# Performance work log

Hardware: AMD Instinct MI355X
Metric: run time of the kernel (lower is better)

The kernel has to match this reference:

```python
import jax, jax.numpy as jnp
import numpy as np
from jax import lax

B = 16
D_OUT = 1024      # flattened face-encoder latent
D_HID = 512       # config.mesh_conv.latent_channels
D_TEX = 16        # config.tex_features (output texture channels)
D_INTER = 32      # d_tex_inter
TEX = 256         # config.tex_dim
K = 3             # kernel_size
N0 = D_INTER * D_INTER * K * K   # first (inter->inter) filter size
N1 = D_TEX * D_INTER * K * K     # last (inter->tex) filter size
D_FLT9 = N0 + N1                 # = 13824


def setup_inputs() -> dict:
    key = jax.random.key(0)
    ks = jax.random.split(key, 8)
    return {
        "z_face": jax.random.normal(ks[0], (B, D_OUT), jnp.float32),
        "tex_data": jax.random.normal(ks[1], (1, D_INTER, TEX, TEX), jnp.float32),
        "W1": jax.random.normal(ks[2], (D_HID, D_OUT), jnp.float32) * 0.02,
        "b1": jnp.zeros((D_HID,), jnp.float32),
        "W2": jax.random.normal(ks[3], (D_HID, D_HID), jnp.float32) * 0.02,
        "b2": jnp.zeros((D_HID,), jnp.float32),
        "W3": jax.random.normal(ks[4], (D_FLT9, D_HID), jnp.float32) * 0.02,
        "b3": jnp.zeros((D_FLT9,), jnp.float32),
    }


def _lrelu(x):
    return jnp.where(x >= 0, x, 0.2 * x)


def reference(z_face, tex_data, W1, b1, W2, b2, W3, b3):
    # proj_w MLP: Linear -> LeakyReLU(0.2) -> Linear -> LeakyReLU(0.2) -> Linear
    h = _lrelu(z_face @ W1.T + b1)
    h = _lrelu(h @ W2.T + b2)
    weights = h @ W3.T + b3                      # [B, D_FLT9]

    flt0 = weights[:, :N0].reshape(B, D_INTER, D_INTER, K, K)   # inter->inter
    flt1 = weights[:, N0:].reshape(B, D_TEX, D_INTER, K, K)     # inter->tex

    pad_l = (K - 1) // 2
    pad_r = K - 1 - pad_l
    pad = [(pad_l, pad_r), (pad_l, pad_r)]

    def per_sample(w0, w1):
        # tex_data is shared across the batch (shape [1, D_INTER, TEX, TEX])
        x = lax.conv_general_dilated(tex_data, w0, (1, 1), pad)  # [1, D_INTER, TEX, TEX]
        x = _lrelu(x)
        x = lax.conv_general_dilated(x, w1, (1, 1), pad)         # [1, D_TEX, TEX, TEX]
        return x[0]

    out = jax.vmap(per_sample)(flt0, flt1)       # [B, D_TEX, TEX, TEX]
    return out
```

## Files before the change

kernel.cpp:

```cpp
#include <hip/hip_runtime.h>
#include <hip/hip_bf16.h>

#define BATCH 16
#define D_OUT 1024
#define D_HID 512
#define D_FLT 13824
#define N0Q 9216
#define TW 14
#define TH 14
#define NXT 19
#define NYT 19
#define NB 2

typedef __attribute__((ext_vector_type(8))) short bf16x8;
typedef __attribute__((ext_vector_type(4))) float f32x4;

__device__ __forceinline__ float lrelu(float x) { return x >= 0.f ? x : 0.2f * x; }
__device__ __forceinline__ ushort f2bf(float x) {
  unsigned u = __float_as_uint(x);
  u += 0x7FFFu + ((u >> 16) & 1u);
  return (ushort)(u >> 16);
}
__device__ __forceinline__ float dot4(float4 a, float4 b) {
  return a.x * b.x + a.y * b.y + a.z * b.z + a.w * b.w;
}
__device__ __forceinline__ bf16x8 cvt8(const float* p) {
  float4 lo = *(const float4*)p;
  float4 hi = *(const float4*)(p + 4);
  bf16x8 r;
  r[0] = (short)f2bf(lo.x); r[1] = (short)f2bf(lo.y);
  r[2] = (short)f2bf(lo.z); r[3] = (short)f2bf(lo.w);
  r[4] = (short)f2bf(hi.x); r[5] = (short)f2bf(hi.y);
  r[6] = (short)f2bf(hi.z); r[7] = (short)f2bf(hi.w);
  return r;
}

__global__ void fc1_tex_kernel(const float* __restrict__ z, const float* __restrict__ W1,
                               const float* __restrict__ b1, float* __restrict__ h1,
                               const float* __restrict__ tex, ushort* __restrict__ texT) {
  int tid = threadIdx.x;
  if (blockIdx.x < 256) {
    int p = blockIdx.x * 256 + tid;
    unsigned pk[16];
    #pragma unroll
    for (int i = 0; i < 16; ++i) {
      ushort lo = f2bf(tex[(2 * i) * 65536 + p]);
      ushort hi = f2bf(tex[(2 * i + 1) * 65536 + p]);
      pk[i] = (unsigned)lo | ((unsigned)hi << 16);
    }
    uint4* dst = (uint4*)&texT[(size_t)p * 32];
    #pragma unroll
    for (int qq = 0; qq < 4; ++qq) {
      uint4 v; v.x = pk[qq * 4]; v.y = pk[qq * 4 + 1]; v.z = pk[qq * 4 + 2]; v.w = pk[qq * 4 + 3];
      dst[qq] = v;
    }
    return;
  }
  int w = tid >> 6, lane = tid & 63;
  int wid = (blockIdx.x - 256) * 4 + w;
  int b = wid >> 7, j0 = (wid & 127) * 4;
  const float4* zv = (const float4*)(z + b * D_OUT);
  float4 zr[4];
  #pragma unroll
  for (int i = 0; i < 4; ++i) zr[i] = zv[lane + i * 64];
  float s[4];
  #pragma unroll
  for (int jj = 0; jj < 4; ++jj) {
    const float4* wv = (const float4*)(W1 + (j0 + jj) * D_OUT);
    float t = 0.f;
    #pragma unroll
    for (int i = 0; i < 4; ++i) t += dot4(zr[i], wv[lane + i * 64]);
    s[jj] = t;
  }
  #pragma unroll
  for (int jj = 0; jj < 4; ++jj) {
    #pragma unroll
    for (int off = 32; off; off >>= 1) s[jj] += __shfl_xor(s[jj], off);
  }
  if (lane == 0) {
    #pragma unroll
    for (int jj = 0; jj < 4; ++jj)
      h1[b * D_HID + j0 + jj] = lrelu(s[jj] + b1[j0 + jj]);
  }
}

__global__ void fc2_kernel(const float* __restrict__ in, const float* __restrict__ W,
                           const float* __restrict__ bias, float* __restrict__ out) {
  int tid = threadIdx.x;
  int w = tid >> 6, lane = tid & 63;
  int wid = blockIdx.x * 4 + w;
  int b = wid >> 7, j0 = (wid & 127) * 4;
  const float4* iv = (const float4*)(in + b * D_HID);
  float4 ir[2];
  #pragma unroll
  for (int i = 0; i < 2; ++i) ir[i] = iv[lane + i * 64];
  float s[4];
  #pragma unroll
  for (int jj = 0; jj < 4; ++jj) {
    const float4* wv = (const float4*)(W + (j0 + jj) * D_HID);
    float t = 0.f;
    #pragma unroll
    for (int i = 0; i < 2; ++i) t += dot4(ir[i], wv[lane + i * 64]);
    s[jj] = t;
  }
  #pragma unroll
  for (int jj = 0; jj < 4; ++jj) {
    #pragma unroll
    for (int off = 32; off; off >>= 1) s[jj] += __shfl_xor(s[jj], off);
  }
  if (lane == 0) {
    #pragma unroll
    for (int jj = 0; jj < 4; ++jj)
      out[b * D_HID + j0 + jj] = lrelu(s[jj] + bias[j0 + jj]);
  }
}

__global__ __launch_bounds__(256) void fc3_mfma(const float* __restrict__ h2,
                                                const float* __restrict__ W3,
                                                const float* __restrict__ b3,
                                                ushort* __restrict__ wbf) {
  const int tid = threadIdx.x;
  const int w = tid >> 6, lane = tid & 63;
  const int jn = lane & 15, q = lane >> 4;
  int t = blockIdx.x * 4 + w;
  int jbase, dstbase, ci0;
  if (t < 576) {
    int kp = t >> 6, rem = t & 63;
    int co = rem >> 1;
    ci0 = (rem & 1) * 16;
    jbase = co * 288 + kp;
    dstbase = kp * 1024 + co * 32 + ci0;
  } else {
    int t2 = t - 576;
    int kp = t2 >> 5, rem = t2 & 31;
    int co = rem >> 1;
    ci0 = (rem & 1) * 16;
    jbase = N0Q + co * 288 + kp;
    dstbase = N0Q + kp * 512 + co * 32 + ci0;
  }
  const float* wrow = W3 + (size_t)(jbase + (ci0 + jn) * 9) * D_HID;
  const float* hrow = h2 + jn * D_HID;
  f32x4 acc = {0.f, 0.f, 0.f, 0.f};
  #pragma unroll
  for (int ks = 0; ks < 16; ++ks) {
    int k0 = ks * 32 + q * 8;
    bf16x8 a = cvt8(wrow + k0);
    bf16x8 bv = cvt8(hrow + k0);
    acc = __builtin_amdgcn_mfma_f32_16x16x32_bf16(a, bv, acc, 0, 0, 0);
  }
  ushort4 o;
  o.x = f2bf(acc[0] + b3[jbase + (ci0 + q * 4 + 0) * 9]);
  o.y = f2bf(acc[1] + b3[jbase + (ci0 + q * 4 + 1) * 9]);
  o.z = f2bf(acc[2] + b3[jbase + (ci0 + q * 4 + 2) * 9]);
  o.w = f2bf(acc[3] + b3[jbase + (ci0 + q * 4 + 3) * 9]);
  *(ushort4*)&wbf[(size_t)jn * D_FLT + dstbase + q * 4] = o;
}

__global__ __launch_bounds__(256, 4) void conv_mfma(const ushort* __restrict__ texT,
                                                    const ushort* __restrict__ wbf,
                                                    float* __restrict__ out) {
  extern __shared__ ushort sm[];
  ushort* texs  = sm;
  ushort* inter = sm + 10368;
  const int tid = threadIdx.x;
  const int w = tid >> 6, lane = tid & 63;
  const int jn = lane & 15, q = lane >> 4;
  const int tx0 = blockIdx.x * TW, ty0 = blockIdx.y * TH;

  for (int i = tid; i < 1296; i += 256) {
    int row = i / 72, c = i - row * 72;
    int px = c >> 2, j = c & 3;
    int gy = ty0 - 2 + row, gx = tx0 - 2 + px;
    int4 v; v.x = 0; v.y = 0; v.z = 0; v.w = 0;
    if (gy >= 0 && gy < 256 && gx >= 0 && gx < 256)
      v = ((const int4*)texT)[(gy * 256 + gx) * 4 + j];
    ((int4*)texs)[row * 72 + px * 4 + ((j + (px >> 1)) & 3)] = v;
  }
  __syncthreads();

  const int s1 = 4 * w;

  #pragma unroll 1
  for (int bb = 0; bb < NB; ++bb) {
    const int b = blockIdx.z * NB + bb;
    const ushort* wb = wbf + (size_t)b * D_FLT;

    if (bb) __syncthreads();

    #pragma unroll 1
    for (int h = 0; h < 2; ++h) {
      bf16x8 a0[9];
      #pragma unroll
      for (int kp = 0; kp < 9; ++kp)
        a0[kp] = *(const bf16x8*)&wb[(kp * 32 + h * 16 + jn) * 32 + q * 8];

      f32x4 acc[4];
      #pragma unroll
      for (int i = 0; i < 4; ++i) acc[i] = f32x4{0.f, 0.f, 0.f, 0.f};
      #pragma unroll
      for (int kyp = 0; kyp < 6; ++kyp) {
        const ushort* trow = &texs[(s1 + kyp) * 576];
        bf16x8 Bf[3];
        #pragma unroll
        for (int kx = 0; kx < 3; ++kx) {
          int p = jn + kx;
          Bf[kx] = *(const bf16x8*)&trow[p * 32 + ((q + (p >> 1)) & 3) * 8];
        }
        #pragma unroll
        for (int i = 0; i < 4; ++i) {
          int ky = kyp - i;
          if (ky >= 0 && ky < 3) {
            #pragma unroll
            for (int kx = 0; kx < 3; ++kx)
              acc[i] = __builtin_amdgcn_mfma_f32_16x16x32_bf16(a0[ky * 3 + kx], Bf[kx], acc[i], 0, 0, 0);
          }
        }
      }
      #pragma unroll
      for (int i = 0; i < 4; ++i) {
        int r = s1 + i;
        int gy1 = ty0 - 1 + r, gx1 = tx0 - 1 + jn;
        bool inimg = (gy1 >= 0 && gy1 < 256 && gx1 >= 0 && gx1 < 256);
        ushort4 p0;
        p0.x = f2bf(lrelu(acc[i][0])); p0.y = f2bf(lrelu(acc[i][1]));
        p0.z = f2bf(lrelu(acc[i][2])); p0.w = f2bf(lrelu(acc[i][3]));
        if (!inimg) { p0.x = p0.y = p0.z = p0.w = 0; }
        *(ushort4*)&inter[r * 512 + jn * 32 +
                          (((2 * h + (q >> 1) + (jn >> 1)) & 3) * 8) + (q & 1) * 4] = p0;
      }
      __builtin_amdgcn_sched_barrier(0);
    }

    bf16x8 a1[9];
    #pragma unroll
    for (int kp = 0; kp < 9; ++kp)
      a1[kp] = *(const bf16x8*)&wb[N0Q + (kp * 16 + jn) * 32 + q * 8];
    __syncthreads();

    {
      const int s2 = 4 * w;
      f32x4 c[4];
      #pragma unroll
      for (int i = 0; i < 4; ++i) c[i] = f32x4{0.f, 0.f, 0.f, 0.f};
      #pragma unroll
      for (int kyp = 0; kyp < 6; ++kyp) {
        int ir = s2 + kyp; if (ir > 15) ir = 15;
        const ushort* irow = &inter[ir * 512];
        bf16x8 Bf[3];
        #pragma unroll
        for (int kx = 0; kx < 3; ++kx) {
          int p = jn + kx;
          Bf[kx] = *(const bf16x8*)&irow[p * 32 + ((q + (p >> 1)) & 3) * 8];
        }
        #pragma unroll
        for (int i = 0; i < 4; ++i) {
          int ky = kyp - i;
          if (ky >= 0 && ky < 3) {
            #pragma unroll
            for (int kx = 0; kx < 3; ++kx)
              c[i] = __builtin_amdgcn_mfma_f32_16x16x32_bf16(a1[ky * 3 + kx], Bf[kx], c[i], 0, 0, 0);
          }
        }
      }
      int gx = tx0 + jn;
      if (jn < TW && gx < 256) {
        #pragma unroll
        for (int i = 0; i < 4; ++i) {
          int ro = s2 + i;
          int gy = ty0 + ro;
          if (ro < TH && gy < 256) {
            #pragma unroll
            for (int ci = 0; ci < 4; ++ci) {
              int co = q * 4 + ci;
              out[(((size_t)b * 16 + co) * 256 + gy) * 256 + gx] = c[i][ci];
            }
          }
        }
      }
    }
  }
}

extern "C" void kernel_launch(void* const* d_in, const int* in_sizes, int n_in,
                              void* d_out, int out_size, void* d_ws, size_t ws_size,
                              hipStream_t stream) {
  const float* z   = (const float*)d_in[0];
  const float* tex = (const float*)d_in[1];
  const float* W1  = (const float*)d_in[2];
  const float* b1  = (const float*)d_in[3];
  const float* W2  = (const float*)d_in[4];
  const float* b2  = (const float*)d_in[5];
  const float* W3  = (const float*)d_in[6];
  const float* b3  = (const float*)d_in[7];
  float* out = (float*)d_out;

  float*  h1   = (float*)d_ws;
  float*  h2   = (float*)((char*)d_ws + 32768);
  ushort* wbf  = (ushort*)((char*)d_ws + 65536);
  ushort* texT = (ushort*)((char*)d_ws + 507904);

  fc1_tex_kernel<<<768, 256, 0, stream>>>(z, W1, b1, h1, tex, texT);
  fc2_kernel<<<512, 256, 0, stream>>>(h1, W2, b2, h2);
  fc3_mfma<<<216, 256, 0, stream>>>(h2, W3, b3, wbf);

  dim3 grid(NXT, NYT, BATCH / NB);
  conv_mfma<<<grid, 256, (10368 + 8192 + 128) * sizeof(ushort), stream>>>(texT, wbf, out);
}
```

Measured before the change: 84.94 us.

## Double-buffer intermediate conv tile and pipeline second conv across batches

Splits the intermediate activation buffer into two shared-memory buffers so the second convolution for the previous batch runs in the same phase as the first convolution for the current batch, with one barrier per batch. Each block now processes four batches instead of two, reusing the staged texture tile more and halving the grid's z dimension. Launch bounds drop to two blocks per CU to allow more registers. The tradeoff is more LDS per block and fewer resident waves, which may reduce latency hiding.

```diff
diff --git a/kernel.cpp b/kernel.cpp
--- a/kernel.cpp
+++ b/kernel.cpp
@@ -10,7 +10,7 @@
 #define TH 14
 #define NXT 19
 #define NYT 19
-#define NB 2
+#define NB 4
 
 typedef __attribute__((ext_vector_type(8))) short bf16x8;
 typedef __attribute__((ext_vector_type(4))) float f32x4;
@@ -156,12 +156,13 @@
   *(ushort4*)&wbf[(size_t)jn * D_FLT + dstbase + q * 4] = o;
 }
 
-__global__ __launch_bounds__(256, 4) void conv_mfma(const ushort* __restrict__ texT,
+__global__ __launch_bounds__(256, 2) void conv_mfma(const ushort* __restrict__ texT,
                                                     const ushort* __restrict__ wbf,
                                                     float* __restrict__ out) {
   extern __shared__ ushort sm[];
-  ushort* texs  = sm;
-  ushort* inter = sm + 10368;
+  ushort* texs   = sm;
+  ushort* interA = sm + 10368;
+  ushort* interB = sm + 18688;
   const int tid = threadIdx.x;
   const int w = tid >> 6, lane = tid & 63;
   const int jn = lane & 15, q = lane >> 4;
@@ -184,8 +185,55 @@
   for (int bb = 0; bb < NB; ++bb) {
     const int b = blockIdx.z * NB + bb;
     const ushort* wb = wbf + (size_t)b * D_FLT;
-
-    if (bb) __syncthreads();
+    ushort* intw = (bb & 1) ? interB : interA;
+
+    if (bb > 0) {
+      const int bp = b - 1;
+      const ushort* wbp = wbf + (size_t)bp * D_FLT;
+      const ushort* intr = (bb & 1) ? interA : interB;
+      bf16x8 a1[9];
+      #pragma unroll
+      for (int kp = 0; kp < 9; ++kp)
+        a1[kp] = *(const bf16x8*)&wbp[N0Q + (kp * 16 + jn) * 32 + q * 8];
+      f32x4 c[4];
+      #pragma unroll
+      for (int i = 0; i < 4; ++i) c[i] = f32x4{0.f, 0.f, 0.f, 0.f};
+      #pragma unroll
+      for (int kyp = 0; kyp < 6; ++kyp) {
+        int ir = s1 + kyp; if (ir > 15) ir = 15;
+        const ushort* irow = &intr[ir * 512];
+        bf16x8 Bf[3];
+        #pragma unroll
+        for (int kx = 0; kx < 3; ++kx) {
+          int p = jn + kx;
+          Bf[kx] = *(const bf16x8*)&irow[p * 32 + ((q + (p >> 1)) & 3) * 8];
+        }
+        #pragma unroll
+        for (int i = 0; i < 4; ++i) {
+          int ky = kyp - i;
+          if (ky >= 0 && ky < 3) {
+            #pragma unroll
+            for (int kx = 0; kx < 3; ++kx)
+              c[i] = __builtin_amdgcn_mfma_f32_16x16x32_bf16(a1[ky * 3 + kx], Bf[kx], c[i], 0, 0, 0);
+          }
+        }
+      }
+      int gx = tx0 + jn;
+      if (jn < TW && gx < 256) {
+        #pragma unroll
+        for (int i = 0; i < 4; ++i) {
+          int ro = s1 + i;
+          int gy = ty0 + ro;
+          if (ro < TH && gy < 256) {
+            #pragma unroll
+            for (int ci = 0; ci < 4; ++ci) {
+              int co = q * 4 + ci;
+              out[(((size_t)bp * 16 + co) * 256 + gy) * 256 + gx] = c[i][ci];
+            }
+          }
+        }
+      }
+    }
 
     #pragma unroll 1
     for (int h = 0; h < 2; ++h) {
@@ -193,7 +241,6 @@
       #pragma unroll
       for (int kp = 0; kp < 9; ++kp)
         a0[kp] = *(const bf16x8*)&wb[(kp * 32 + h * 16 + jn) * 32 + q * 8];
-
       f32x4 acc[4];
       #pragma unroll
       for (int i = 0; i < 4; ++i) acc[i] = f32x4{0.f, 0.f, 0.f, 0.f};
@@ -225,55 +272,55 @@
         p0.x = f2bf(lrelu(acc[i][0])); p0.y = f2bf(lrelu(acc[i][1]));
         p0.z = f2bf(lrelu(acc[i][2])); p0.w = f2bf(lrelu(acc[i][3]));
         if (!inimg) { p0.x = p0.y = p0.z = p0.w = 0; }
-        *(ushort4*)&inter[r * 512 + jn * 32 +
-                          (((2 * h + (q >> 1) + (jn >> 1)) & 3) * 8) + (q & 1) * 4] = p0;
-      }
-      __builtin_amdgcn_sched_barrier(0);
-    }
-
+        *(ushort4*)&intw[r * 512 + jn * 32 +
+                         (((2 * h + (q >> 1) + (jn >> 1)) & 3) * 8) + (q & 1) * 4] = p0;
+      }
+    }
+    __syncthreads();
+  }
+
+  {
+    const int bp = blockIdx.z * NB + NB - 1;
+    const ushort* wbp = wbf + (size_t)bp * D_FLT;
+    const ushort* intr = interB;
     bf16x8 a1[9];
     #pragma unroll
     for (int kp = 0; kp < 9; ++kp)
-      a1[kp] = *(const bf16x8*)&wb[N0Q + (kp * 16 + jn) * 32 + q * 8];
-    __syncthreads();
-
-    {
-      const int s2 = 4 * w;
-      f32x4 c[4];
-      #pragma unroll
-      for (int i = 0; i < 4; ++i) c[i] = f32x4{0.f, 0.f, 0.f, 0.f};
-      #pragma unroll
-      for (int kyp = 0; kyp < 6; ++kyp) {
-        int ir = s2 + kyp; if (ir > 15) ir = 15;
-        const ushort* irow = &inter[ir * 512];
-        bf16x8 Bf[3];
-        #pragma unroll
-        for (int kx = 0; kx < 3; ++kx) {
-          int p = jn + kx;
-          Bf[kx] = *(const bf16x8*)&irow[p * 32 + ((q + (p >> 1)) & 3) * 8];
-        }
-        #pragma unroll
-        for (int i = 0; i < 4; ++i) {
-          int ky = kyp - i;
-          if (ky >= 0 && ky < 3) {
-            #pragma unroll
-            for (int kx = 0; kx < 3; ++kx)
-              c[i] = __builtin_amdgcn_mfma_f32_16x16x32_bf16(a1[ky * 3 + kx], Bf[kx], c[i], 0, 0, 0);
-          }
-        }
-      }
-      int gx = tx0 + jn;
-      if (jn < TW && gx < 256) {
-        #pragma unroll
-        for (int i = 0; i < 4; ++i) {
-          int ro = s2 + i;
-          int gy = ty0 + ro;
-          if (ro < TH && gy < 256) {
-            #pragma unroll
-            for (int ci = 0; ci < 4; ++ci) {
-              int co = q * 4 + ci;
-              out[(((size_t)b * 16 + co) * 256 + gy) * 256 + gx] = c[i][ci];
-            }
+      a1[kp] = *(const bf16x8*)&wbp[N0Q + (kp * 16 + jn) * 32 + q * 8];
+    f32x4 c[4];
+    #pragma unroll
+    for (int i = 0; i < 4; ++i) c[i] = f32x4{0.f, 0.f, 0.f, 0.f};
+    #pragma unroll
+    for (int kyp = 0; kyp < 6; ++kyp) {
+      int ir = s1 + kyp; if (ir > 15) ir = 15;
+      const ushort* irow = &intr[ir * 512];
+      bf16x8 Bf[3];
+      #pragma unroll
+      for (int kx = 0; kx < 3; ++kx) {
+        int p = jn + kx;
+        Bf[kx] = *(const bf16x8*)&irow[p * 32 + ((q + (p >> 1)) & 3) * 8];
+      }
+      #pragma unroll
+      for (int i = 0; i < 4; ++i) {
+        int ky = kyp - i;
+        if (ky >= 0 && ky < 3) {
+          #pragma unroll
+          for (int kx = 0; kx < 3; ++kx)
+            c[i] = __builtin_amdgcn_mfma_f32_16x16x32_bf16(a1[ky * 3 + kx], Bf[kx], c[i], 0, 0, 0);
+        }
+      }
+    }
+    int gx = tx0 + jn;
+    if (jn < TW && gx < 256) {
+      #pragma unroll
+      for (int i = 0; i < 4; ++i) {
+        int ro = s1 + i;
+        int gy = ty0 + ro;
+        if (ro < TH && gy < 256) {
+          #pragma unroll
+          for (int ci = 0; ci < 4; ++ci) {
+            int co = q * 4 + ci;
+            out[(((size_t)bp * 16 + co) * 256 + gy) * 256 + gx] = c[i][ci];
           }
         }
       }
@@ -304,5 +351,5 @@
   fc3_mfma<<<216, 256, 0, stream>>>(h2, W3, b3, wbf);
 
   dim3 grid(NXT, NYT, BATCH / NB);
-  conv_mfma<<<grid, 256, (10368 + 8192 + 128) * sizeof(ushort), stream>>>(texT, wbf, out);
-}
+  conv_mfma<<<grid, 256, (10368 + 8320 + 8320) * sizeof(ushort), stream>>>(texT, wbf, out);
+}
```

New measurement: 92.33 us. 1.09x slower.
